# Kernel optimization log

Measured on AMD Instinct MI355X. Metric: run time of the kernel, lower is better.

## Reference

```python
import jax, jax.numpy as jnp
import numpy as np

CHANNELS = 32
HIDDEN = 1024
LAYERS = 8
NODE_TYPES = 7
N_NODES = 500_000
N_EDGES = 2_000_000
NUM_GRAPHS = 1024


def setup_inputs() -> dict:
    key = jax.random.key(0)
    ks = jax.random.split(key, 8)
    nodes = jax.random.randint(ks[0], (N_NODES,), 0, NODE_TYPES)
    sources = jax.random.randint(ks[1], (N_EDGES,), 0, N_NODES)
    targets = jax.random.randint(ks[2], (N_EDGES,), 0, N_NODES)
    # sorted graph ids covering all NUM_GRAPHS graphs (no empty graphs)
    batch = (jnp.arange(N_NODES) * NUM_GRAPHS) // N_NODES
    emb = jax.random.normal(ks[3], (NODE_TYPES, CHANNELS), dtype=jnp.float32)
    # xavier-normal-ish init for the 8 layers x {out, back} 32x32 convs
    xavier_std = (2.0 / (CHANNELS + CHANNELS)) ** 0.5
    conv_w = jax.random.normal(ks[4], (LAYERS, 2, CHANNELS, CHANNELS), dtype=jnp.float32) * xavier_std
    hidden_w = jax.random.normal(ks[5], (CHANNELS, HIDDEN), dtype=jnp.float32) * 0.05
    hidden_b = jax.random.normal(ks[6], (HIDDEN,), dtype=jnp.float32) * 0.05
    out_w = jax.random.normal(ks[7], (HIDDEN, 1), dtype=jnp.float32) * 0.05
    return dict(nodes=nodes, sources=sources, targets=targets, batch=batch,
                emb=emb, conv_w=conv_w, hidden_w=hidden_w, hidden_b=hidden_b,
                out_w=out_w)


def reference(nodes, sources, targets, batch, emb, conv_w, hidden_w, hidden_b, out_w):
    n = nodes.shape[0]
    ones_e = jnp.ones(sources.shape[0], dtype=jnp.float32)
    # norm = 1 / (1 + in-degree), norm_t = 1 / (1 + out-degree)  [N,1]
    norm = (1.0 / (1.0 + jax.ops.segment_sum(ones_e, targets, num_segments=n)))[:, None]
    norm_t = (1.0 / (1.0 + jax.ops.segment_sum(ones_e, sources, num_segments=n)))[:, None]
    node_counts = jax.ops.segment_sum(jnp.ones(n, dtype=jnp.float32), batch,
                                      num_segments=NUM_GRAPHS)

    x = emb[nodes]  # [N, C]

    def conv(x, s, t, nrm, w):
        # x.index_add(0, t, x[s]) -> x + scatter_add of gathered source feats
        agg = nrm * (x + jax.ops.segment_sum(x[s], t, num_segments=n))
        return jax.nn.relu(agg @ w)

    for l in range(LAYERS):
        x = x + conv(x, sources, targets, norm, conv_w[l, 0]) \
              + conv(x, targets, sources, norm_t, conv_w[l, 1])

    # mean pooling per graph
    g = jax.ops.segment_sum(x, batch, num_segments=NUM_GRAPHS) / node_counts[:, None]
    h = jax.nn.relu(g @ hidden_w + hidden_b)
    return (h @ out_w).squeeze(-1)  # [NUM_GRAPHS]
```

## Files before the change

### kernel.cpp

```cpp
#include <hip/hip_runtime.h>

#define CHANNELS 32
#define HIDDEN 1024
#define LAYERS 8
#define NRANGE 8

typedef __attribute__((ext_vector_type(8))) short short8;
typedef __attribute__((ext_vector_type(4))) float float4v;

__device__ __forceinline__ short f2bf_rne(float f) {
    union { float f; unsigned u; } v; v.f = f;
    unsigned r = v.u + 0x7fffu + ((v.u >> 16) & 1u);
    return (short)(r >> 16);
}
__device__ __forceinline__ float bf2f(short h) {
    union { float f; unsigned u; } v; v.u = ((unsigned)(unsigned short)h) << 16;
    return v.f;
}
__device__ __forceinline__ float bfu2f(unsigned short h) {
    union { float f; unsigned u; } v; v.u = ((unsigned)h) << 16;
    return v.f;
}


__global__ __launch_bounds__(256)
void deg_range_kernel(const int* __restrict__ src, const int* __restrict__ tgt,
                      int* __restrict__ deg2, int n_nodes, int n_edges, int rsh) {
    int r = blockIdx.x & (NRANGE - 1);
    int chunk = blockIdx.x >> 3;
    int base = chunk * 2048;
#pragma unroll
    for (int j = 0; j < 8; j++) {
        int e = base + j * 256 + threadIdx.x;
        if (e < n_edges) {
            int t = __builtin_nontemporal_load(tgt + e);
            int s = __builtin_nontemporal_load(src + e);
            if ((t >> rsh) == r) atomicAdd(&deg2[t], 1);
            if ((s >> rsh) == r) atomicAdd(&deg2[n_nodes + s], 1);
        }
    }
}


__global__ __launch_bounds__(256)
void scan_pass1(const int* __restrict__ deg, int* __restrict__ bs, int n) {
    __shared__ int sh[256];
    int t = threadIdx.x;
    int base = blockIdx.x * 2048 + t * 8;
    int s = 0;
#pragma unroll
    for (int j = 0; j < 8; j++) { int idx = base + j; if (idx < n) s += deg[idx]; }
    sh[t] = s; __syncthreads();
    for (int st = 128; st > 0; st >>= 1) { if (t < st) sh[t] += sh[t + st]; __syncthreads(); }
    if (t == 0) bs[blockIdx.x] = sh[0];
}

__global__ void scan_pass2(int* __restrict__ bs, int nb) {
    __shared__ int sh[1024];
    int t = threadIdx.x;
    int v = (t < nb) ? bs[t] : 0;
    sh[t] = v; __syncthreads();
    for (int off = 1; off < 1024; off <<= 1) {
        int u = (t >= off) ? sh[t - off] : 0; __syncthreads();
        sh[t] += u; __syncthreads();
    }
    if (t < nb) bs[t] = sh[t] - v;
}

__global__ __launch_bounds__(256)
void scan_pass3(const int* __restrict__ deg, const int* __restrict__ bs,
                int* __restrict__ off, int n) {
    __shared__ int sh[256];
    int t = threadIdx.x;
    int base = blockIdx.x * 2048 + t * 8;
    int v[8]; int s = 0;
#pragma unroll
    for (int j = 0; j < 8; j++) { int idx = base + j; v[j] = (idx < n) ? deg[idx] : 0; s += v[j]; }
    sh[t] = s; __syncthreads();
    for (int st = 1; st < 256; st <<= 1) {
        int u = (t >= st) ? sh[t - st] : 0; __syncthreads();
        sh[t] += u; __syncthreads();
    }
    int acc = bs[blockIdx.x] + sh[t] - s;
#pragma unroll
    for (int j = 0; j < 8; j++) { int idx = base + j; if (idx < n) off[idx] = acc; acc += v[j]; }
}


__global__ __launch_bounds__(256)
void scatter_range_kernel(const int* __restrict__ src, const int* __restrict__ tgt,
                          int* __restrict__ cur2, int* __restrict__ nbr,
                          int n_nodes, int n_edges, int rsh) {
    int r = blockIdx.x & (NRANGE - 1);
    int chunk = blockIdx.x >> 3;
    int base = chunk * 2048;
#pragma unroll
    for (int j = 0; j < 8; j++) {
        int e = base + j * 256 + threadIdx.x;
        if (e < n_edges) {
            int t = __builtin_nontemporal_load(tgt + e);
            int s = __builtin_nontemporal_load(src + e);
            if ((t >> rsh) == r) { int p = atomicAdd(&cur2[t], 1);           nbr[p] = s; }
            if ((s >> rsh) == r) { int q = atomicAdd(&cur2[n_nodes + s], 1); nbr[q] = t; }
        }
    }
}


__global__ __launch_bounds__(256)
void init_kernel(const int* __restrict__ nodes, const float* __restrict__ emb,
                 const int* __restrict__ deg2,
                 float* __restrict__ x, unsigned short* __restrict__ xg,
                 float* __restrict__ norm, float* __restrict__ norm_t, int n_nodes) {
    int gid = blockIdx.x * blockDim.x + threadIdx.x;
    int i = gid >> 5, c = gid & 31;
    if (i >= n_nodes) return;
    float v = emb[nodes[i] * CHANNELS + c];
    x[gid] = v;
    xg[gid] = (unsigned short)f2bf_rne(v);
    if (c == 0) {
        norm[i]   = 1.0f / (1.0f + (float)deg2[i]);
        norm_t[i] = 1.0f / (1.0f + (float)deg2[n_nodes + i]);
    }
}


__global__ void counts_kernel(const int* __restrict__ batch, float* __restrict__ counts,
                              int n_nodes, int n_graphs) {
    int b = blockIdx.x * blockDim.x + threadIdx.x;
    if (b >= n_graphs) return;
    int lo = 0, hi = n_nodes;
    while (lo < hi) { int mid = (lo + hi) >> 1; if (batch[mid] < b) lo = mid + 1; else hi = mid; }
    int s = lo;
    lo = 0; hi = n_nodes;
    while (lo < hi) { int mid = (lo + hi) >> 1; if (batch[mid] < b + 1) lo = mid + 1; else hi = mid; }
    counts[b] = (float)(lo - s);
}


__global__ __launch_bounds__(256)
void layer_mfma(const int* __restrict__ off2, const int* __restrict__ nbr,
                const float* __restrict__ wbase,
                const float* __restrict__ norm, const float* __restrict__ norm_t,
                float* __restrict__ x,
                const unsigned short* __restrict__ xgin,
                unsigned short* __restrict__ xgout,
                int n_nodes, int n_edges) {
    __shared__ short A1h[64][32], A1l[64][32], A2h[64][32], A2l[64][32];
    __shared__ short W0h[32][32], W0l[32][32], W1h[32][32], W1l[32][32];
    __shared__ int offIn[65], offOut[65];

    int tid = threadIdx.x;
    int nodeblock = blockIdx.x * 64;

    for (int idx = tid; idx < CHANNELS * CHANNELS; idx += 256) {
        int k = idx >> 5, n = idx & 31;
        float w0 = wbase[idx];
        float w1 = wbase[CHANNELS * CHANNELS + idx];
        short h0 = f2bf_rne(w0); W0h[n][k] = h0; W0l[n][k] = f2bf_rne(w0 - bf2f(h0));
        short h1 = f2bf_rne(w1); W1h[n][k] = h1; W1l[n][k] = f2bf_rne(w1 - bf2f(h1));
    }
    if (tid < 65) {
        int idx = nodeblock + tid;
        offIn[tid]  = (idx <= n_nodes) ? off2[idx] : n_edges;
        int idx2 = n_nodes + idx;
        offOut[tid] = (idx2 < 2 * n_nodes) ? off2[idx2] : 2 * n_edges;
    }
    __syncthreads();

    int c = tid & 31, g = tid >> 5;

    int bi_c, d1_c, bo_c, d2_c, nbl1_c, nbl2_c, node_c;
    float xv_c;
    {
        int local = g;
        node_c = nodeblock + local;
        bi_c = offIn[local];  d1_c = offIn[local + 1] - bi_c;
        bo_c = offOut[local]; d2_c = offOut[local + 1] - bo_c;
        nbl1_c = (c < d1_c) ? nbr[bi_c + c] : 0;
        nbl2_c = (c < d2_c) ? nbr[bo_c + c] : 0;
        xv_c = (node_c < n_nodes) ? x[node_c * CHANNELS + c] : 0.f;
    }

    for (int pass = 0; pass < 8; pass++) {
        int bi_n = 0, d1_n = 0, bo_n = 0, d2_n = 0, nbl1_n = 0, nbl2_n = 0, node_n = 0;
        float xv_n = 0.f;
        if (pass < 7) {
            int local = (pass + 1) * 8 + g;
            node_n = nodeblock + local;
            bi_n = offIn[local];  d1_n = offIn[local + 1] - bi_n;
            bo_n = offOut[local]; d2_n = offOut[local + 1] - bo_n;
            nbl1_n = (c < d1_n) ? nbr[bi_n + c] : 0;
            nbl2_n = (c < d2_n) ? nbr[bo_n + c] : 0;
            xv_n = (node_n < n_nodes) ? x[node_n * CHANNELS + c] : 0.f;
        }

        int local = pass * 8 + g;
        int i = node_c;
        int self = (i < n_nodes) ? i : 0;

        int m1 = d1_c < 32 ? d1_c : 32;
        int m2 = d2_c < 32 ? d2_c : 32;
        int mm = m1 > m2 ? m1 : m2;

        float a1 = 0.f, a2 = 0.f;
        for (int j = 0; j < mm; j += 4) {
            int p0 = __shfl(nbl1_c, (j)     & 31, 32);
            int p1 = __shfl(nbl1_c, (j + 1) & 31, 32);
            int p2 = __shfl(nbl1_c, (j + 2) & 31, 32);
            int p3 = __shfl(nbl1_c, (j + 3) & 31, 32);
            int q0 = __shfl(nbl2_c, (j)     & 31, 32);
            int q1 = __shfl(nbl2_c, (j + 1) & 31, 32);
            int q2 = __shfl(nbl2_c, (j + 2) & 31, 32);
            int q3 = __shfl(nbl2_c, (j + 3) & 31, 32);
            p0 = (j     < m1) ? p0 : self;
            p1 = (j + 1 < m1) ? p1 : self;
            p2 = (j + 2 < m1) ? p2 : self;
            p3 = (j + 3 < m1) ? p3 : self;
            q0 = (j     < m2) ? q0 : self;
            q1 = (j + 1 < m2) ? q1 : self;
            q2 = (j + 2 < m2) ? q2 : self;
            q3 = (j + 3 < m2) ? q3 : self;
            float u0 = bfu2f(xgin[p0 * CHANNELS + c]);
            float u1 = bfu2f(xgin[p1 * CHANNELS + c]);
            float u2 = bfu2f(xgin[p2 * CHANNELS + c]);
            float u3 = bfu2f(xgin[p3 * CHANNELS + c]);
            float w0 = bfu2f(xgin[q0 * CHANNELS + c]);
            float w1 = bfu2f(xgin[q1 * CHANNELS + c]);
            float w2 = bfu2f(xgin[q2 * CHANNELS + c]);
            float w3 = bfu2f(xgin[q3 * CHANNELS + c]);
            a1 += (j     < m1) ? u0 : 0.f;
            a1 += (j + 1 < m1) ? u1 : 0.f;
            a1 += (j + 2 < m1) ? u2 : 0.f;
            a1 += (j + 3 < m1) ? u3 : 0.f;
            a2 += (j     < m2) ? w0 : 0.f;
            a2 += (j + 1 < m2) ? w1 : 0.f;
            a2 += (j + 2 < m2) ? w2 : 0.f;
            a2 += (j + 3 < m2) ? w3 : 0.f;
        }
        for (int e = bi_c + 32; e < bi_c + d1_c; e++) a1 += bfu2f(xgin[nbr[e] * CHANNELS + c]);
        for (int e = bo_c + 32; e < bo_c + d2_c; e++) a2 += bfu2f(xgin[nbr[e] * CHANNELS + c]);

        if (i < n_nodes) {
            float n1 = norm[i], n2 = norm_t[i];
            a1 = n1 * (xv_c + a1);
            a2 = n2 * (xv_c + a2);
            short h1 = f2bf_rne(a1);
            A1h[local][c] = h1; A1l[local][c] = f2bf_rne(a1 - bf2f(h1));
            short h2 = f2bf_rne(a2);
            A2h[local][c] = h2; A2l[local][c] = f2bf_rne(a2 - bf2f(h2));
        } else {
            A1h[local][c] = 0; A1l[local][c] = 0;
            A2h[local][c] = 0; A2l[local][c] = 0;
        }

        bi_c = bi_n; d1_c = d1_n; bo_c = bo_n; d2_c = d2_n;
        nbl1_c = nbl1_n; nbl2_c = nbl2_n; xv_c = xv_n; node_c = node_n;
    }
    __syncthreads();

    int wv = tid >> 6, lane = tid & 63;
    int m = lane & 15, quad = lane >> 4;
    int row0 = wv * 16;

    short8 a1h = *(const short8*)&A1h[row0 + m][quad * 8];
    short8 a1l = *(const short8*)&A1l[row0 + m][quad * 8];
    short8 a2h = *(const short8*)&A2h[row0 + m][quad * 8];
    short8 a2l = *(const short8*)&A2l[row0 + m][quad * 8];

    float4v dd[4];
#pragma unroll
    for (int h = 0; h < 2; h++) {
        int n0 = h * 16 + m;
        short8 b0h = *(const short8*)&W0h[n0][quad * 8];
        short8 b0l = *(const short8*)&W0l[n0][quad * 8];
        short8 b1h = *(const short8*)&W1h[n0][quad * 8];
        short8 b1l = *(const short8*)&W1l[n0][quad * 8];
        float4v d1 = {0.f, 0.f, 0.f, 0.f};
        d1 = __builtin_amdgcn_mfma_f32_16x16x32_bf16(a1h, b0h, d1, 0, 0, 0);
        d1 = __builtin_amdgcn_mfma_f32_16x16x32_bf16(a1l, b0h, d1, 0, 0, 0);
        d1 = __builtin_amdgcn_mfma_f32_16x16x32_bf16(a1h, b0l, d1, 0, 0, 0);
        float4v d2 = {0.f, 0.f, 0.f, 0.f};
        d2 = __builtin_amdgcn_mfma_f32_16x16x32_bf16(a2h, b1h, d2, 0, 0, 0);
        d2 = __builtin_amdgcn_mfma_f32_16x16x32_bf16(a2l, b1h, d2, 0, 0, 0);
        d2 = __builtin_amdgcn_mfma_f32_16x16x32_bf16(a2h, b1l, d2, 0, 0, 0);
        dd[h * 2] = d1; dd[h * 2 + 1] = d2;
    }

#pragma unroll
    for (int h = 0; h < 2; h++) {
        float4v d1 = dd[h * 2], d2 = dd[h * 2 + 1];
#pragma unroll
        for (int r = 0; r < 4; r++) {
            int local = row0 + quad * 4 + r;
            int node = nodeblock + local;
            if (node < n_nodes) {
                int col = h * 16 + m;
                float v = x[node * CHANNELS + col] + fmaxf(d1[r], 0.f) + fmaxf(d2[r], 0.f);
                x[node * CHANNELS + col] = v;
                xgout[node * CHANNELS + col] = (unsigned short)f2bf_rne(v);
            }
        }
    }
}


#define POOL_CHUNK 2048

__global__ __launch_bounds__(256)
void pool_kernel(const int* __restrict__ batch, const float* __restrict__ x,
                 float* __restrict__ g, int n_nodes) {
    int c = threadIdx.x & 31;
    int r = threadIdx.x >> 5;
    int base = blockIdx.x * POOL_CHUNK;
    float acc = 0.f;
    int cur = -1;
    for (int it = 0; it < POOL_CHUNK / 8; it++) {
        int node = base + it * 8 + r;
        if (node >= n_nodes) break;
        int b = batch[node];
        if (b != cur) {
            if (cur >= 0) atomicAdd(&g[cur * CHANNELS + c], acc);
            acc = 0.f;
            cur = b;
        }
        acc += x[node * CHANNELS + c];
    }
    if (cur >= 0) atomicAdd(&g[cur * CHANNELS + c], acc);
}


__global__ __launch_bounds__(256)
void mlp_kernel(const float* __restrict__ g, const float* __restrict__ counts,
                const float* __restrict__ hidden_w, const float* __restrict__ hidden_b,
                const float* __restrict__ out_w, float* __restrict__ out) {
    __shared__ float grow[CHANNELS];
    __shared__ float red[256];
    int graph = blockIdx.x;
    int tid = threadIdx.x;
    if (tid < CHANNELS) grow[tid] = g[graph * CHANNELS + tid] / counts[graph];
    __syncthreads();
    float partial = 0.f;
    for (int q = 0; q < HIDDEN / 256; q++) {
        int j = q * 256 + tid;
        float h = hidden_b[j];
#pragma unroll
        for (int k = 0; k < CHANNELS; k++) h += grow[k] * hidden_w[k * HIDDEN + j];
        partial += fmaxf(h, 0.f) * out_w[j];
    }
    red[tid] = partial;
    __syncthreads();
    for (int s = 128; s > 0; s >>= 1) {
        if (tid < s) red[tid] += red[tid + s];
        __syncthreads();
    }
    if (tid == 0) out[graph] = red[0];
}


extern "C" void kernel_launch(void* const* d_in, const int* in_sizes, int n_in,
                              void* d_out, int out_size, void* d_ws, size_t ws_size,
                              hipStream_t stream) {
    const int*   nodes    = (const int*)d_in[0];
    const int*   sources  = (const int*)d_in[1];
    const int*   targets  = (const int*)d_in[2];
    const int*   batch    = (const int*)d_in[3];
    const float* emb      = (const float*)d_in[4];
    const float* conv_w   = (const float*)d_in[5];
    const float* hidden_w = (const float*)d_in[6];
    const float* hidden_b = (const float*)d_in[7];
    const float* out_w    = (const float*)d_in[8];
    float* out = (float*)d_out;

    const int n_nodes  = in_sizes[0];
    const int n_edges  = in_sizes[1];
    const int n_graphs = out_size;
    const int n2 = 2 * n_nodes;

    int rsh = 0;
    while (((n_nodes - 1) >> rsh) >= NRANGE) rsh++;

    char* ws = (char*)d_ws;
    float*          x      = (float*)ws;          ws += (size_t)n_nodes * CHANNELS * 4;
    unsigned short* xg0    = (unsigned short*)ws; ws += (size_t)n_nodes * CHANNELS * 2;
    unsigned short* xg1    = (unsigned short*)ws; ws += (size_t)n_nodes * CHANNELS * 2;
    float* norm   = (float*)ws; ws += (size_t)n_nodes * 4;
    float* norm_t = (float*)ws; ws += (size_t)n_nodes * 4;
    int*   deg2   = (int*)ws;   ws += (size_t)n2 * 4;
    int*   off2   = (int*)ws;   ws += (size_t)n2 * 4;
    int*   cur2   = (int*)ws;   ws += (size_t)n2 * 4;
    int*   nbr    = (int*)ws;   ws += (size_t)2 * n_edges * 4;
    int*   bsums  = (int*)ws;   ws += 4096;
    float* g      = (float*)ws; ws += (size_t)n_graphs * CHANNELS * 4;
    float* counts = (float*)ws; ws += (size_t)n_graphs * 4;

    hipMemsetAsync(deg2, 0, (size_t)n2 * 4, stream);
    hipMemsetAsync(g, 0, (size_t)n_graphs * CHANNELS * 4, stream);

    int echunks = (n_edges + 2047) / 2048;

    deg_range_kernel<<<echunks * NRANGE, 256, 0, stream>>>(sources, targets, deg2,
                                                           n_nodes, n_edges, rsh);

    int nblk = (n2 + 2047) / 2048;
    scan_pass1<<<nblk, 256, 0, stream>>>(deg2, bsums, n2);
    scan_pass2<<<1, 1024, 0, stream>>>(bsums, nblk);
    scan_pass3<<<nblk, 256, 0, stream>>>(deg2, bsums, off2, n2);

    hipMemcpyAsync(cur2, off2, (size_t)n2 * 4, hipMemcpyDeviceToDevice, stream);
    scatter_range_kernel<<<echunks * NRANGE, 256, 0, stream>>>(sources, targets, cur2, nbr,
                                                               n_nodes, n_edges, rsh);

    int node_thr = n_nodes * CHANNELS;
    init_kernel<<<(node_thr + 255) / 256, 256, 0, stream>>>(nodes, emb, deg2, x, xg0,
                                                            norm, norm_t, n_nodes);
    counts_kernel<<<(n_graphs + 255) / 256, 256, 0, stream>>>(batch, counts, n_nodes, n_graphs);

    unsigned short* xgin = xg0; unsigned short* xgout = xg1;
    int lblocks = (n_nodes + 63) / 64;
    for (int l = 0; l < LAYERS; l++) {
        const float* wbase = conv_w + (size_t)l * 2 * CHANNELS * CHANNELS;
        layer_mfma<<<lblocks, 256, 0, stream>>>(off2, nbr, wbase, norm, norm_t,
                                                x, xgin, xgout, n_nodes, n_edges);
        unsigned short* tmp = xgin; xgin = xgout; xgout = tmp;
    }

    int pool_blocks = (n_nodes + POOL_CHUNK - 1) / POOL_CHUNK;
    pool_kernel<<<pool_blocks, 256, 0, stream>>>(batch, x, g, n_nodes);
    mlp_kernel<<<n_graphs, 256, 0, stream>>>(g, counts, hidden_w, hidden_b, out_w, out);
}
```

Measured before the change: 1.729 ms.

## Process two nodes per warp-group in layer gather and split scatter into 16 ranges

The layer kernel's gather loop now handles two nodes at once per 32-lane group, interleaving their neighbor loads to put more independent memory requests in flight, with the next pair prefetched. Node assignment changes from strided (pass*8+g) to contiguous (g*8+k) within the block. The CSR scatter is split into two launches covering 16 node ranges, so each pass touches a smaller slice of the counters and neighbor array, aiming for better cache locality of the atomics. The cost is higher register pressure and one extra pass over the edge arrays.

```diff
diff --git a/kernel.cpp b/kernel.cpp
--- a/kernel.cpp
+++ b/kernel.cpp
@@ -90,8 +90,8 @@
 __global__ __launch_bounds__(256)
 void scatter_range_kernel(const int* __restrict__ src, const int* __restrict__ tgt,
                           int* __restrict__ cur2, int* __restrict__ nbr,
-                          int n_nodes, int n_edges, int rsh) {
-    int r = blockIdx.x & (NRANGE - 1);
+                          int n_nodes, int n_edges, int rsh, int rbase) {
+    int r = rbase + (blockIdx.x & (NRANGE - 1));
     int chunk = blockIdx.x >> 3;
     int base = chunk * 2048;
 #pragma unroll
@@ -138,6 +138,21 @@
 }
 
 
+__device__ __forceinline__ void load_node_state(
+    const int* __restrict__ nbr, const float* __restrict__ x,
+    const int* offIn, const int* offOut,
+    int nodeblock, int local, int c, int n_nodes,
+    int& node, int& bi, int& d1, int& bo, int& d2,
+    int& nb1, int& nb2, float& xv)
+{
+    node = nodeblock + local;
+    bi = offIn[local];  d1 = offIn[local + 1] - bi;
+    bo = offOut[local]; d2 = offOut[local + 1] - bo;
+    nb1 = (c < d1) ? nbr[bi + c] : 0;
+    nb2 = (c < d2) ? nbr[bo + c] : 0;
+    xv = (node < n_nodes) ? x[node * CHANNELS + c] : 0.f;
+}
+
 __global__ __launch_bounds__(256)
 void layer_mfma(const int* __restrict__ off2, const int* __restrict__ nbr,
                 const float* __restrict__ wbase,
@@ -169,93 +184,100 @@
     __syncthreads();
 
     int c = tid & 31, g = tid >> 5;
-
-    int bi_c, d1_c, bo_c, d2_c, nbl1_c, nbl2_c, node_c;
-    float xv_c;
-    {
-        int local = g;
-        node_c = nodeblock + local;
-        bi_c = offIn[local];  d1_c = offIn[local + 1] - bi_c;
-        bo_c = offOut[local]; d2_c = offOut[local + 1] - bo_c;
-        nbl1_c = (c < d1_c) ? nbr[bi_c + c] : 0;
-        nbl2_c = (c < d2_c) ? nbr[bo_c + c] : 0;
-        xv_c = (node_c < n_nodes) ? x[node_c * CHANNELS + c] : 0.f;
-    }
-
-    for (int pass = 0; pass < 8; pass++) {
-        int bi_n = 0, d1_n = 0, bo_n = 0, d2_n = 0, nbl1_n = 0, nbl2_n = 0, node_n = 0;
-        float xv_n = 0.f;
-        if (pass < 7) {
-            int local = (pass + 1) * 8 + g;
-            node_n = nodeblock + local;
-            bi_n = offIn[local];  d1_n = offIn[local + 1] - bi_n;
-            bo_n = offOut[local]; d2_n = offOut[local + 1] - bo_n;
-            nbl1_n = (c < d1_n) ? nbr[bi_n + c] : 0;
-            nbl2_n = (c < d2_n) ? nbr[bo_n + c] : 0;
-            xv_n = (node_n < n_nodes) ? x[node_n * CHANNELS + c] : 0.f;
-        }
-
-        int local = pass * 8 + g;
-        int i = node_c;
-        int self = (i < n_nodes) ? i : 0;
-
-        int m1 = d1_c < 32 ? d1_c : 32;
-        int m2 = d2_c < 32 ? d2_c : 32;
-        int mm = m1 > m2 ? m1 : m2;
-
-        float a1 = 0.f, a2 = 0.f;
+    int baseL = g * 8;
+
+    int nodeA, biA, d1A, boA, d2A, nbA1, nbA2; float xvA;
+    int nodeB, biB, d1B, boB, d2B, nbB1, nbB2; float xvB;
+    load_node_state(nbr, x, offIn, offOut, nodeblock, baseL,     c, n_nodes,
+                    nodeA, biA, d1A, boA, d2A, nbA1, nbA2, xvA);
+    load_node_state(nbr, x, offIn, offOut, nodeblock, baseL + 1, c, n_nodes,
+                    nodeB, biB, d1B, boB, d2B, nbB1, nbB2, xvB);
+
+    for (int it = 0; it < 4; it++) {
+        int nodeA_n = 0, biA_n = 0, d1A_n = 0, boA_n = 0, d2A_n = 0, nbA1_n = 0, nbA2_n = 0;
+        int nodeB_n = 0, biB_n = 0, d1B_n = 0, boB_n = 0, d2B_n = 0, nbB1_n = 0, nbB2_n = 0;
+        float xvA_n = 0.f, xvB_n = 0.f;
+        if (it < 3) {
+            load_node_state(nbr, x, offIn, offOut, nodeblock, baseL + 2 * it + 2, c, n_nodes,
+                            nodeA_n, biA_n, d1A_n, boA_n, d2A_n, nbA1_n, nbA2_n, xvA_n);
+            load_node_state(nbr, x, offIn, offOut, nodeblock, baseL + 2 * it + 3, c, n_nodes,
+                            nodeB_n, biB_n, d1B_n, boB_n, d2B_n, nbB1_n, nbB2_n, xvB_n);
+        }
+
+        int selfA = (nodeA < n_nodes) ? nodeA : 0;
+        int selfB = (nodeB < n_nodes) ? nodeB : 0;
+        int m1A = d1A < 32 ? d1A : 32;
+        int m2A = d2A < 32 ? d2A : 32;
+        int m1B = d1B < 32 ? d1B : 32;
+        int m2B = d2B < 32 ? d2B : 32;
+        int mm = m1A > m2A ? m1A : m2A;
+        int mb = m1B > m2B ? m1B : m2B;
+        mm = mm > mb ? mm : mb;
+
+        float a1A = 0.f, a2A = 0.f, a1B = 0.f, a2B = 0.f;
         for (int j = 0; j < mm; j += 4) {
-            int p0 = __shfl(nbl1_c, (j)     & 31, 32);
-            int p1 = __shfl(nbl1_c, (j + 1) & 31, 32);
-            int p2 = __shfl(nbl1_c, (j + 2) & 31, 32);
-            int p3 = __shfl(nbl1_c, (j + 3) & 31, 32);
-            int q0 = __shfl(nbl2_c, (j)     & 31, 32);
-            int q1 = __shfl(nbl2_c, (j + 1) & 31, 32);
-            int q2 = __shfl(nbl2_c, (j + 2) & 31, 32);
-            int q3 = __shfl(nbl2_c, (j + 3) & 31, 32);
-            p0 = (j     < m1) ? p0 : self;
-            p1 = (j + 1 < m1) ? p1 : self;
-            p2 = (j + 2 < m1) ? p2 : self;
-            p3 = (j + 3 < m1) ? p3 : self;
-            q0 = (j     < m2) ? q0 : self;
-            q1 = (j + 1 < m2) ? q1 : self;
-            q2 = (j + 2 < m2) ? q2 : self;
-            q3 = (j + 3 < m2) ? q3 : self;
-            float u0 = bfu2f(xgin[p0 * CHANNELS + c]);
-            float u1 = bfu2f(xgin[p1 * CHANNELS + c]);
-            float u2 = bfu2f(xgin[p2 * CHANNELS + c]);
-            float u3 = bfu2f(xgin[p3 * CHANNELS + c]);
-            float w0 = bfu2f(xgin[q0 * CHANNELS + c]);
-            float w1 = bfu2f(xgin[q1 * CHANNELS + c]);
-            float w2 = bfu2f(xgin[q2 * CHANNELS + c]);
-            float w3 = bfu2f(xgin[q3 * CHANNELS + c]);
-            a1 += (j     < m1) ? u0 : 0.f;
-            a1 += (j + 1 < m1) ? u1 : 0.f;
-            a1 += (j + 2 < m1) ? u2 : 0.f;
-            a1 += (j + 3 < m1) ? u3 : 0.f;
-            a2 += (j     < m2) ? w0 : 0.f;
-            a2 += (j + 1 < m2) ? w1 : 0.f;
-            a2 += (j + 2 < m2) ? w2 : 0.f;
-            a2 += (j + 3 < m2) ? w3 : 0.f;
-        }
-        for (int e = bi_c + 32; e < bi_c + d1_c; e++) a1 += bfu2f(xgin[nbr[e] * CHANNELS + c]);
-        for (int e = bo_c + 32; e < bo_c + d2_c; e++) a2 += bfu2f(xgin[nbr[e] * CHANNELS + c]);
-
-        if (i < n_nodes) {
-            float n1 = norm[i], n2 = norm_t[i];
-            a1 = n1 * (xv_c + a1);
-            a2 = n2 * (xv_c + a2);
+            int pA[4], qA[4], pB[4], qB[4];
+#pragma unroll
+            for (int u = 0; u < 4; u++) {
+                int jj = (j + u) & 31;
+                pA[u] = __shfl(nbA1, jj, 32);
+                qA[u] = __shfl(nbA2, jj, 32);
+                pB[u] = __shfl(nbB1, jj, 32);
+                qB[u] = __shfl(nbB2, jj, 32);
+                pA[u] = (j + u < m1A) ? pA[u] : selfA;
+                qA[u] = (j + u < m2A) ? qA[u] : selfA;
+                pB[u] = (j + u < m1B) ? pB[u] : selfB;
+                qB[u] = (j + u < m2B) ? qB[u] : selfB;
+            }
+            float vA1[4], vA2[4], vB1[4], vB2[4];
+#pragma unroll
+            for (int u = 0; u < 4; u++) {
+                vA1[u] = bfu2f(xgin[pA[u] * CHANNELS + c]);
+                vA2[u] = bfu2f(xgin[qA[u] * CHANNELS + c]);
+                vB1[u] = bfu2f(xgin[pB[u] * CHANNELS + c]);
+                vB2[u] = bfu2f(xgin[qB[u] * CHANNELS + c]);
+            }
+#pragma unroll
+            for (int u = 0; u < 4; u++) {
+                a1A += (j + u < m1A) ? vA1[u] : 0.f;
+                a2A += (j + u < m2A) ? vA2[u] : 0.f;
+                a1B += (j + u < m1B) ? vB1[u] : 0.f;
+                a2B += (j + u < m2B) ? vB2[u] : 0.f;
+            }
+        }
+        for (int e = biA + 32; e < biA + d1A; e++) a1A += bfu2f(xgin[nbr[e] * CHANNELS + c]);
+        for (int e = boA + 32; e < boA + d2A; e++) a2A += bfu2f(xgin[nbr[e] * CHANNELS + c]);
+        for (int e = biB + 32; e < biB + d1B; e++) a1B += bfu2f(xgin[nbr[e] * CHANNELS + c]);
+        for (int e = boB + 32; e < boB + d2B; e++) a2B += bfu2f(xgin[nbr[e] * CHANNELS + c]);
+
+        int localA = baseL + 2 * it, localB = localA + 1;
+        if (nodeA < n_nodes) {
+            float a1 = norm[nodeA] * (xvA + a1A);
+            float a2 = norm_t[nodeA] * (xvA + a2A);
             short h1 = f2bf_rne(a1);
-            A1h[local][c] = h1; A1l[local][c] = f2bf_rne(a1 - bf2f(h1));
+            A1h[localA][c] = h1; A1l[localA][c] = f2bf_rne(a1 - bf2f(h1));
             short h2 = f2bf_rne(a2);
-            A2h[local][c] = h2; A2l[local][c] = f2bf_rne(a2 - bf2f(h2));
+            A2h[localA][c] = h2; A2l[localA][c] = f2bf_rne(a2 - bf2f(h2));
         } else {
-            A1h[local][c] = 0; A1l[local][c] = 0;
-            A2h[local][c] = 0; A2l[local][c] = 0;
-        }
-
-        bi_c = bi_n; d1_c = d1_n; bo_c = bo_n; d2_c = d2_n;
-        nbl1_c = nbl1_n; nbl2_c = nbl2_n; xv_c = xv_n; node_c = node_n;
+            A1h[localA][c] = 0; A1l[localA][c] = 0;
+            A2h[localA][c] = 0; A2l[localA][c] = 0;
+        }
+        if (nodeB < n_nodes) {
+            float a1 = norm[nodeB] * (xvB + a1B);
+            float a2 = norm_t[nodeB] * (xvB + a2B);
+            short h1 = f2bf_rne(a1);
+            A1h[localB][c] = h1; A1l[localB][c] = f2bf_rne(a1 - bf2f(h1));
+            short h2 = f2bf_rne(a2);
+            A2h[localB][c] = h2; A2l[localB][c] = f2bf_rne(a2 - bf2f(h2));
+        } else {
+            A1h[localB][c] = 0; A1l[localB][c] = 0;
+            A2h[localB][c] = 0; A2l[localB][c] = 0;
+        }
+
+        nodeA = nodeA_n; biA = biA_n; d1A = d1A_n; boA = boA_n; d2A = d2A_n;
+        nbA1 = nbA1_n; nbA2 = nbA2_n; xvA = xvA_n;
+        nodeB = nodeB_n; biB = biB_n; d1B = d1B_n; boB = boB_n; d2B = d2B_n;
+        nbB1 = nbB1_n; nbB2 = nbB2_n; xvB = xvB_n;
     }
     __syncthreads();
 
@@ -377,8 +399,10 @@
     const int n_graphs = out_size;
     const int n2 = 2 * n_nodes;
 
-    int rsh = 0;
-    while (((n_nodes - 1) >> rsh) >= NRANGE) rsh++;
+    int rsh8 = 0;
+    while (((n_nodes - 1) >> rsh8) >= 8) rsh8++;
+    int rsh16 = 0;
+    while (((n_nodes - 1) >> rsh16) >= 16) rsh16++;
 
     char* ws = (char*)d_ws;
     float*          x      = (float*)ws;          ws += (size_t)n_nodes * CHANNELS * 4;
@@ -400,7 +424,7 @@
     int echunks = (n_edges + 2047) / 2048;
 
     deg_range_kernel<<<echunks * NRANGE, 256, 0, stream>>>(sources, targets, deg2,
-                                                           n_nodes, n_edges, rsh);
+                                                           n_nodes, n_edges, rsh8);
 
     int nblk = (n2 + 2047) / 2048;
     scan_pass1<<<nblk, 256, 0, stream>>>(deg2, bsums, n2);
@@ -409,7 +433,9 @@
 
     hipMemcpyAsync(cur2, off2, (size_t)n2 * 4, hipMemcpyDeviceToDevice, stream);
     scatter_range_kernel<<<echunks * NRANGE, 256, 0, stream>>>(sources, targets, cur2, nbr,
-                                                               n_nodes, n_edges, rsh);
+                                                               n_nodes, n_edges, rsh16, 0);
+    scatter_range_kernel<<<echunks * NRANGE, 256, 0, stream>>>(sources, targets, cur2, nbr,
+                                                               n_nodes, n_edges, rsh16, 8);
 
     int node_thr = n_nodes * CHANNELS;
     init_kernel<<<(node_thr + 255) / 256, 256, 0, stream>>>(nodes, emb, deg2, x, xg0,
```

After: 1.919 ms. 1.11x slower.
